# Kernel optimization log

Measured on AMD Instinct MI355X. Metric: run time of the kernel, lower is better.

The kernel has to match this reference:

```python
import jax, jax.numpy as jnp
import numpy as np
import math

N, E, D, H, EH, DEPTH = 50000, 800000, 128, 128, 16, 3
RATIO = 0.5
BN_SCALE = 1.0 / math.sqrt(1.0 + 1e-5)  # eval-mode BatchNorm1d: running mean 0, var 1
NEG_SLOPE = 0.01  # leaky_relu default


def setup_inputs() -> dict:
    key = jax.random.key(0)
    ks = jax.random.split(key, 16)
    s = lambda k, shape: jax.random.normal(k, shape, dtype=jnp.float32) * 0.05
    return {
        "x": jax.random.normal(ks[0], (N, D), dtype=jnp.float32),
        "edge_index": jax.random.randint(ks[1], (2, E), 0, N, dtype=jnp.int32),
        "edge_attr": jax.random.uniform(ks[2], (E, EH), dtype=jnp.float32),
        "We_w": s(ks[3], (EH, 1)), "We_b": s(ks[4], (1,)),
        "Wdown": s(ks[5], (DEPTH + 1, H, H)), "bdown": s(ks[6], (DEPTH + 1, H)),
        "Wpool": s(ks[7], (DEPTH, H)),
        "Wup": s(ks[8], (DEPTH, H, H)), "bup": s(ks[9], (DEPTH, H)),
        "gnorm": 1.0 + s(ks[10], (DEPTH + 1, H)), "bnorm": s(ks[11], (DEPTH + 1, H)),
        "Wr": s(ks[12], (D, D)), "br": s(ks[13], (D,)),
        "gr": 1.0 + s(ks[14], (D,)), "brn": s(ks[15], (D,)),
    }


def _bn(x, g, b):
    # eval-mode BatchNorm1d with running_mean=0, running_var=1
    return x * (g * BN_SCALE) + b


def _lrelu(x):
    return jnp.where(x > 0, x, NEG_SLOPE * x)


def _gcn(x, src, dst, w, W, b, fill):
    # PyG GCNConv: add self-loops (fill=1.0, improved -> 2.0), symmetric norm
    n = x.shape[0]
    h = x @ W  # [n, H]
    deg = jax.ops.segment_sum(w, dst, num_segments=n) + fill
    dinv = jax.lax.rsqrt(deg)
    coef = dinv[src] * w * dinv[dst]  # [E]
    agg = jax.ops.segment_sum(coef[:, None] * h[src], dst, num_segments=n)
    return agg + (fill / deg)[:, None] * h + b  # self-loop norm = fill/deg


def _topk_pool(x, src, dst, w, p, k):
    # PyG TopKPooling: score = tanh(x.p/||p||), keep top-k, scale kept x by score,
    # filter edges to kept nodes (masked edges kept at fixed length with weight 0)
    n = x.shape[0]
    score = jnp.tanh((x @ p) / jnp.linalg.norm(p))
    vals, perm = jax.lax.top_k(score, k)
    xp = x[perm] * vals[:, None]
    pos = jnp.full((n,), -1, dtype=jnp.int32).at[perm].set(jnp.arange(k, dtype=jnp.int32))
    ns, nd = pos[src], pos[dst]
    valid = (ns >= 0) & (nd >= 0)
    return (xp, jnp.where(valid, ns, 0), jnp.where(valid, nd, 0),
            jnp.where(valid, w, 0.0), perm)


def reference(x, edge_index, edge_attr, We_w, We_b, Wdown, bdown, Wpool, Wup, bup,
              gnorm, bnorm, Wr, br, gr, brn):
    src, dst = edge_index[0], edge_index[1]
    # edge embedding + min/max normalization
    ew = edge_attr @ We_w[:, 0] + We_b[0]  # [E]
    ew = ew - jnp.min(ew)
    ew = ew / (jnp.max(ew) + 1e-7)
    h = _bn(x, gnorm[0], bnorm[0])
    h = _lrelu(_gcn(h, src, dst, ew, Wdown[0], bdown[0], 1.0))
    xs, es, perms = [h], [(src, dst, ew)], []
    for i in range(DEPTH):
        k = int(math.ceil(RATIO * h.shape[0]))
        h, src, dst, ew, perm = _topk_pool(h, src, dst, ew, Wpool[i], k)
        h = _bn(h, gnorm[i + 1], bnorm[i + 1])
        h = _gcn(h, src, dst, ew, Wdown[i + 1], bdown[i + 1], 1.0)
        if i < DEPTH - 1:
            h = _lrelu(h)
            xs.append(h)
            es.append((src, dst, ew))
        perms.append(perm)
    for i in range(DEPTH):
        j = DEPTH - 1 - i
        res = xs[j]
        src, dst, ew = es[j]
        up = jnp.zeros_like(res).at[perms[j]].set(h)  # scatter unpool
        h = _gcn(res + up, src, dst, ew, Wup[i], bup[i], 2.0)  # improved=True -> fill 2
        if i < DEPTH - 1:
            h = _lrelu(h)
    g = jnp.sum(h, axis=0, keepdims=True)  # global_add_pool, single graph
    g = g @ Wr + br
    return _bn(g, gr, brn)
```

## Files before the change

kernel.cpp:

```cpp
#include <hip/hip_runtime.h>
#include <math.h>

#define N0   50000
#define E0   800000
#define HD   128
#define EHD  16
#define KP1  25000
#define KP2  12500
#define KP3  6250
#define BN_SCALE 0.9999950000374997f
#define NEG_SLOPE 0.01f
#define E1C  400000
#define E2C  120000
#define E3C  40000
#define NBE  782
#define CSB  782

#define NBIN   782
#define EPB    6144
#define NBLK   131
#define NBINP  784

typedef int   vi4 __attribute__((ext_vector_type(4)));
typedef float vf4 __attribute__((ext_vector_type(4)));

__device__ __forceinline__ unsigned fenc(float f) {
    unsigned u = __float_as_uint(f);
    return (u & 0x80000000u) ? ~u : (u | 0x80000000u);
}
__device__ __forceinline__ unsigned packbf2(float a, float b) {
    unsigned ua = __float_as_uint(a);
    unsigned ub = __float_as_uint(b);
    ua = (ua + 0x7FFFu + ((ua >> 16) & 1u)) >> 16;
    ub = (ub + 0x7FFFu + ((ub >> 16) & 1u)) >> 16;
    return ua | (ub << 16);
}
__device__ __forceinline__ void bf8_fma(float* acc, uint4 h, float c) {
    acc[0] += c * __uint_as_float(h.x << 16);
    acc[1] += c * __uint_as_float(h.x & 0xFFFF0000u);
    acc[2] += c * __uint_as_float(h.y << 16);
    acc[3] += c * __uint_as_float(h.y & 0xFFFF0000u);
    acc[4] += c * __uint_as_float(h.z << 16);
    acc[5] += c * __uint_as_float(h.z & 0xFFFF0000u);
    acc[6] += c * __uint_as_float(h.w << 16);
    acc[7] += c * __uint_as_float(h.w & 0xFFFF0000u);
}

__global__ void k_edge_ew(const float* __restrict__ ea, const float* __restrict__ Ww,
                          const float* __restrict__ Wb, float* __restrict__ ew,
                          float2* __restrict__ partials, int E) {
    int e = blockIdx.x * 256 + threadIdx.x;
    float mn = 3.4e38f, mx = -3.4e38f;
    if (e < E) {
        const float4* a4 = (const float4*)(ea + (size_t)e * EHD);
        float s = Wb[0];
        #pragma unroll
        for (int q = 0; q < 4; ++q) {
            float4 a = a4[q];
            s += a.x * Ww[q*4+0] + a.y * Ww[q*4+1] + a.z * Ww[q*4+2] + a.w * Ww[q*4+3];
        }
        ew[e] = s;
        mn = s; mx = s;
    }
    #pragma unroll
    for (int off = 32; off > 0; off >>= 1) {
        mn = fminf(mn, __shfl_xor(mn, off));
        mx = fmaxf(mx, __shfl_xor(mx, off));
    }
    __shared__ float smn[4], smx[4];
    int lane = threadIdx.x & 63, wid = threadIdx.x >> 6;
    if (lane == 0) { smn[wid] = mn; smx[wid] = mx; }
    __syncthreads();
    if (threadIdx.x == 0) {
        float a = fminf(fminf(smn[0], smn[1]), fminf(smn[2], smn[3]));
        float b = fmaxf(fmaxf(smx[0], smx[1]), fmaxf(smx[2], smx[3]));
        partials[blockIdx.x] = make_float2(a, b);
    }
}

__global__ void __launch_bounds__(1024)
k_reduce_mm(const float2* __restrict__ partials, int nb, float* __restrict__ mmv) {
    float mn = 3.4e38f, mx = -3.4e38f;
    for (int i = threadIdx.x; i < nb; i += 1024) {
        float2 t = partials[i];
        mn = fminf(mn, t.x); mx = fmaxf(mx, t.y);
    }
    #pragma unroll
    for (int off = 32; off > 0; off >>= 1) {
        mn = fminf(mn, __shfl_xor(mn, off));
        mx = fmaxf(mx, __shfl_xor(mx, off));
    }
    __shared__ float smn[16], smx[16];
    int lane = threadIdx.x & 63, wid = threadIdx.x >> 6;
    if (lane == 0) { smn[wid] = mn; smx[wid] = mx; }
    __syncthreads();
    if (threadIdx.x == 0) {
        for (int w = 1; w < 16; ++w) { mn = fminf(mn, smn[w]); mx = fmaxf(mx, smx[w]); }
        mmv[0] = mn; mmv[1] = mx;
    }
}

__global__ void __launch_bounds__(1024)
k_ew_sortA(float* __restrict__ ew, const float* __restrict__ mmv,
           const int* __restrict__ src, const int* __restrict__ dst,
           uint2* __restrict__ staging, int* __restrict__ cntM,
           int* __restrict__ locOffM, int E) {
    __shared__ uint2 sEnt[EPB];
    __shared__ int   lhist[NBINP];
    __shared__ int   sOff[NBINP];
    __shared__ int   lcur[NBINP];
    __shared__ int   wtot[16];
    int t = threadIdx.x;
    for (int i = t; i < NBINP; i += 1024) lhist[i] = 0;
    __syncthreads();
    float mn = mmv[0];
    float sc = 1.0f / ((mmv[1] - mn) + 1e-7f);
    int base = blockIdx.x * EPB;
    unsigned entx[6], enty[6];
    int bin6[6];
    #pragma unroll
    for (int it = 0; it < 6; ++it) {
        int e = base + it * 1024 + t;
        bin6[it] = -1;
        if (e < E) {
            float w = (ew[e] - mn) * sc;
            ew[e] = w;
            if (w != 0.0f) {
                int d = dst[e];
                bin6[it] = d >> 6;
                entx[it] = (unsigned)src[e] | ((unsigned)(d & 63) << 16);
                enty[it] = __float_as_uint(w);
                atomicAdd(&lhist[bin6[it]], 1);
            }
        }
    }
    __syncthreads();
    {
        int v = (t < NBINP) ? lhist[t] : 0;
        int lane = t & 63, wid = t >> 6;
        int x = v;
        #pragma unroll
        for (int off = 1; off < 64; off <<= 1) {
            int y = __shfl_up(x, off);
            if (lane >= off) x += y;
        }
        if (lane == 63) wtot[wid] = x;
        __syncthreads();
        int wb = 0;
        for (int w = 0; w < wid; ++w) wb += wtot[w];
        int excl = wb + x - v;
        if (t < NBINP) { sOff[t] = excl; lcur[t] = excl; }
    }
    __syncthreads();
    #pragma unroll
    for (int it = 0; it < 6; ++it) {
        if (bin6[it] >= 0) {
            int slot = atomicAdd(&lcur[bin6[it]], 1);
            sEnt[slot] = make_uint2(entx[it], enty[it]);
        }
    }
    __syncthreads();
    int total = sOff[NBIN];
    uint2* dstS = staging + (size_t)blockIdx.x * EPB;
    for (int i = t; i < total; i += 1024) dstS[i] = sEnt[i];
    int* cRow = cntM + blockIdx.x * NBINP;
    int* oRow = locOffM + blockIdx.x * NBINP;
    for (int i = t; i < NBINP; i += 1024) { cRow[i] = lhist[i]; oRow[i] = sOff[i]; }
}

__global__ void __launch_bounds__(1024)
k_bin_scan2(const int* __restrict__ cntM, int* __restrict__ binBase,
            int* __restrict__ rowptrEnd) {
    int t = threadIdx.x;
    int v = 0;
    if (t < NBIN) {
        for (int blk = 0; blk < NBLK; ++blk) v += cntM[blk * NBINP + t];
    }
    int lane = t & 63, wid = t >> 6;
    int xs = v;
    #pragma unroll
    for (int off = 1; off < 64; off <<= 1) {
        int y = __shfl_up(xs, off);
        if (lane >= off) xs += y;
    }
    __shared__ int wsum[16];
    if (lane == 63) wsum[wid] = xs;
    __syncthreads();
    int wb = 0;
    for (int w = 0; w < wid; ++w) wb += wsum[w];
    int excl = wb + xs - v;
    if (t < NBIN) binBase[t] = excl;
    if (t == NBIN - 1) rowptrEnd[0] = excl + v;
}

__global__ void __launch_bounds__(256)
k_binB2(const int* __restrict__ binBase, const int* __restrict__ cntM,
        const int* __restrict__ locOffM, const uint2* __restrict__ staging,
        int2* __restrict__ csr, float* __restrict__ sumW,
        int* __restrict__ rowptr, int n) {
    __shared__ uint2 raw[2048];
    __shared__ int   lhist[64];
    __shared__ int   lcur[64];
    __shared__ float lw[64];
    __shared__ int2  img[2048];
    __shared__ int   wq[4];
    __shared__ int   totalSh;
    int b = blockIdx.x;
    int t = threadIdx.x;
    int base = binBase[b];
    int c = 0, lo = 0;
    if (t < NBLK) { c = cntM[t * NBINP + b]; lo = locOffM[t * NBINP + b]; }
    int lane = t & 63, wid = t >> 6;
    int x = c;
    #pragma unroll
    for (int off = 1; off < 64; off <<= 1) {
        int y = __shfl_up(x, off);
        if (lane >= off) x += y;
    }
    if (lane == 63) wq[wid] = x;
    if (t < 64) { lhist[t] = 0; lw[t] = 0.f; }
    __syncthreads();
    int wb = 0;
    for (int w = 0; w < wid; ++w) wb += wq[w];
    int pos = wb + x - c;
    if (t == 255) totalSh = wb + x;
    __syncthreads();
    int total = min(totalSh, 2048);
    if (t < NBLK && c > 0) {
        const uint2* st = staging + (size_t)t * EPB + lo;
        for (int j = 0; j < c; ++j) {
            int p = pos + j;
            if (p < 2048) raw[p] = st[j];
        }
    }
    __syncthreads();
    for (int i = t; i < total; i += 256) {
        uint2 en = raw[i];
        int dloc = (en.x >> 16) & 63;
        atomicAdd(&lhist[dloc], 1);
        atomicAdd(&lw[dloc], __uint_as_float(en.y));
    }
    __syncthreads();
    if (t < 64) {
        int cc = lhist[t];
        int xs = cc;
        #pragma unroll
        for (int off = 1; off < 64; off <<= 1) {
            int y = __shfl_up(xs, off);
            if (t >= off) xs += y;
        }
        int excl = xs - cc;
        lcur[t] = excl;
        int v = b * 64 + t;
        if (v < n) { rowptr[v] = base + excl; sumW[v] = lw[t]; }
    }
    __syncthreads();
    for (int i = t; i < total; i += 256) {
        uint2 en = raw[i];
        int dloc = (en.x >> 16) & 63;
        int slot = atomicAdd(&lcur[dloc], 1);
        if (slot < 2048) img[slot] = make_int2((int)(en.x & 0xFFFFu), (int)en.y);
    }
    __syncthreads();
    for (int i = t; i < total; i += 256)
        csr[base + i] = img[i];
}

#define GT_ROWS 32
__global__ void __launch_bounds__(256)
k_gemm128(const float* __restrict__ A, const float* __restrict__ W,
          unsigned* __restrict__ Cb, int n,
          const float* __restrict__ gs, const float* __restrict__ gb,
          const float* __restrict__ up_h, const int* __restrict__ up_pos) {
    __shared__ float As[GT_ROWS][132];
    __shared__ float Ws[64][132];
    int tid = threadIdx.x;
    int row0 = blockIdx.x * GT_ROWS;
    int maxr = n - row0;
    {
        #pragma unroll
        for (int it = 0; it < 4; ++it) {
            int idx = it * 256 + tid;
            int r = idx >> 5, q = idx & 31;
            float4 v = make_float4(0.f, 0.f, 0.f, 0.f);
            if (r < maxr) {
                v = ((const float4*)(A + (size_t)(row0 + r) * HD))[q];
                if (up_pos) {
                    int sl = up_pos[row0 + r];
                    if (sl >= 0) {
                        float4 u = ((const float4*)(up_h + (size_t)sl * HD))[q];
                        v.x += u.x; v.y += u.y; v.z += u.z; v.w += u.w;
                    }
                }
                if (gs) {
                    float4 g4 = ((const float4*)gs)[q];
                    float4 b4 = ((const float4*)gb)[q];
                    v.x = v.x * (g4.x * BN_SCALE) + b4.x;
                    v.y = v.y * (g4.y * BN_SCALE) + b4.y;
                    v.z = v.z * (g4.z * BN_SCALE) + b4.z;
                    v.w = v.w * (g4.w * BN_SCALE) + b4.w;
                }
            }
            *(float4*)&As[r][q * 4] = v;
        }
    }
    int cg = tid & 31;
    int rg = tid >> 5;
    float4 acc[4];
    #pragma unroll
    for (int j = 0; j < 4; ++j) acc[j] = make_float4(0.f, 0.f, 0.f, 0.f);
    const float4* W4 = (const float4*)W;
    #pragma unroll
    for (int kb = 0; kb < HD; kb += 64) {
        __syncthreads();
        #pragma unroll
        for (int it = 0; it < 8; ++it) {
            int idx = it * 256 + tid;
            int r = idx >> 5, q = idx & 31;
            *(float4*)&Ws[r][q * 4] = W4[(size_t)(kb + r) * 32 + q];
        }
        __syncthreads();
        #pragma unroll 4
        for (int kk = 0; kk < 64; kk += 4) {
            float4 w0 = *(const float4*)&Ws[kk + 0][cg * 4];
            float4 w1 = *(const float4*)&Ws[kk + 1][cg * 4];
            float4 w2 = *(const float4*)&Ws[kk + 2][cg * 4];
            float4 w3 = *(const float4*)&Ws[kk + 3][cg * 4];
            #pragma unroll
            for (int jj = 0; jj < 4; ++jj) {
                float4 a = *(const float4*)&As[4 * rg + jj][kb + kk];
                acc[jj].x += a.x * w0.x + a.y * w1.x + a.z * w2.x + a.w * w3.x;
                acc[jj].y += a.x * w0.y + a.y * w1.y + a.z * w2.y + a.w * w3.y;
                acc[jj].z += a.x * w0.z + a.y * w1.z + a.z * w2.z + a.w * w3.z;
                acc[jj].w += a.x * w0.w + a.y * w1.w + a.z * w2.w + a.w * w3.w;
            }
        }
    }
    #pragma unroll
    for (int jj = 0; jj < 4; ++jj) {
        int r = 4 * rg + jj;
        if (r < maxr) {
            uint2 pk = make_uint2(packbf2(acc[jj].x, acc[jj].y), packbf2(acc[jj].z, acc[jj].w));
            ((uint2*)(Cb + (size_t)(row0 + r) * 64))[cg] = pk;
        }
    }
}

__global__ void k_sum_scan(const int* __restrict__ cnt, int* __restrict__ bsum, int n,
                           int* __restrict__ totalOut, unsigned* __restrict__ dctr) {
    int base = blockIdx.x * 1024;
    int s = 0;
    #pragma unroll
    for (int it = 0; it < 4; ++it) {
        int i = base + it * 256 + threadIdx.x;
        if (i < n) s += cnt[i];
    }
    __shared__ int ws[4];
    __shared__ int lastFlag;
    int lane = threadIdx.x & 63, wid = threadIdx.x >> 6;
    #pragma unroll
    for (int off = 32; off > 0; off >>= 1) s += __shfl_down(s, off);
    if (lane == 0) ws[wid] = s;
    __syncthreads();
    if (threadIdx.x == 0) {
        __hip_atomic_store(&bsum[blockIdx.x], ws[0] + ws[1] + ws[2] + ws[3],
                           __ATOMIC_RELAXED, __HIP_MEMORY_SCOPE_AGENT);
        unsigned prev = __hip_atomic_fetch_add(dctr, 1u, __ATOMIC_ACQ_REL, __HIP_MEMORY_SCOPE_AGENT);
        lastFlag = (prev == gridDim.x - 1);
    }
    __syncthreads();
    if (!lastFlag) return;
    if (threadIdx.x < 64) {
        int nb = gridDim.x;
        int t = threadIdx.x;
        int v = (t < nb) ? __hip_atomic_load(&bsum[t], __ATOMIC_RELAXED, __HIP_MEMORY_SCOPE_AGENT) : 0;
        int x = v;
        #pragma unroll
        for (int off = 1; off < 64; off <<= 1) {
            int y = __shfl_up(x, off);
            if (t >= off) x += y;
        }
        if (t < nb) bsum[t] = x - v;
        if (t == nb - 1) totalOut[0] = x;
    }
    if (threadIdx.x == 0)
        __hip_atomic_store(dctr, 0u, __ATOMIC_RELAXED, __HIP_MEMORY_SCOPE_AGENT);
}

__global__ void k_chunk_scan(const int* __restrict__ cnt, const int* __restrict__ bo,
                             int* __restrict__ rowptr, int* __restrict__ cursor, int n) {
    __shared__ int wsum[4];
    __shared__ int running;
    int base = blockIdx.x * 1024;
    if (threadIdx.x == 0) running = bo[blockIdx.x];
    __syncthreads();
    int lane = threadIdx.x & 63, wid = threadIdx.x >> 6;
    #pragma unroll
    for (int it = 0; it < 4; ++it) {
        int i = base + it * 256 + threadIdx.x;
        int v = (i < n) ? cnt[i] : 0;
        int x = v;
        #pragma unroll
        for (int off = 1; off < 64; off <<= 1) {
            int y = __shfl_up(x, off);
            if (lane >= off) x += y;
        }
        if (lane == 63) wsum[wid] = x;
        __syncthreads();
        int wb = 0;
        for (int w = 0; w < wid; ++w) wb += wsum[w];
        int excl = running + wb + x - v;
        if (i < n) { rowptr[i] = excl; cursor[i] = excl; }
        __syncthreads();
        if (threadIdx.x == 0) running += wsum[0] + wsum[1] + wsum[2] + wsum[3];
        __syncthreads();
    }
}

__global__ void k_csr_fill(const int* __restrict__ src, const int* __restrict__ dst,
                           const float* __restrict__ w, int* __restrict__ cursor,
                           int2* __restrict__ csr,
                           const int* __restrict__ EinPtr, int EinImm) {
    int Ein = EinPtr ? EinPtr[0] : EinImm;
    int e = blockIdx.x * 256 + threadIdx.x;
    if (e >= Ein) return;
    float wv = w[e];
    if (wv == 0.0f) return;
    int slot = atomicAdd(&cursor[dst[e]], 1);
    csr[slot] = make_int2(src[e], __float_as_int(wv));
}

__global__ void k_deg_dinv(const int* __restrict__ rowptr, const int2* __restrict__ csr,
                           float fill, float* __restrict__ deg, float* __restrict__ dinv, int n) {
    int v = blockIdx.x * 256 + threadIdx.x;
    if (v >= n) return;
    float s = fill;
    int rs = rowptr[v], re = rowptr[v + 1];
    for (int j = rs; j < re; ++j) s += __int_as_float(csr[j].y);
    deg[v] = s;
    dinv[v] = rsqrtf(s);
}

__global__ void k_deg_dinv_d(const float* __restrict__ sumW, float fill,
                             float* __restrict__ deg, float* __restrict__ dinv, int n) {
    int v = blockIdx.x * 256 + threadIdx.x;
    if (v >= n) return;
    float s = fill + sumW[v];
    deg[v] = s;
    dinv[v] = rsqrtf(s);
}

__global__ void __launch_bounds__(256)
k_gcn_gather(const int* __restrict__ rowptr, const int2* __restrict__ csr,
             const float* __restrict__ deg, const float* __restrict__ dinv,
             const unsigned* __restrict__ hWb,
             const float* __restrict__ bias,
             float fill, int n, int lrelu, float* __restrict__ out) {
    int v = blockIdx.x * 4 + (threadIdx.x >> 6);
    int lane = threadIdx.x & 63;
    if (v >= n) return;
    int rs = rowptr[v], re = rowptr[v + 1];
    float dv = dinv[v];
    int quarter = lane >> 4;
    int qi = lane & 15;
    float acc[8];
    #pragma unroll
    for (int i = 0; i < 8; ++i) acc[i] = 0.f;
    for (int base = rs; base < re; base += 64) {
        int idx = base + lane;
        int s_r = 0; float c_r = 0.f;
        if (idx < re) {
            int2 ent = csr[idx];
            s_r = ent.x;
            c_r = dinv[s_r] * __int_as_float(ent.y) * dv;
        }
        int cnt = min(64, re - base);
        int groups = cnt >> 2;
        int t = 0;
        for (; t + 1 < groups; t += 2) {
            int j0 = 4 * t + quarter, j1 = j0 + 4;
            int   s0 = __shfl(s_r, j0); float c0 = __shfl(c_r, j0);
            int   s1 = __shfl(s_r, j1); float c1 = __shfl(c_r, j1);
            uint4 h0 = ((const uint4*)(hWb + (size_t)s0 * 64))[qi];
            uint4 h1 = ((const uint4*)(hWb + (size_t)s1 * 64))[qi];
            bf8_fma(acc, h0, c0);
            bf8_fma(acc, h1, c1);
        }
        for (; t < groups; ++t) {
            int j = 4 * t + quarter;
            int s = __shfl(s_r, j); float c = __shfl(c_r, j);
            uint4 h = ((const uint4*)(hWb + (size_t)s * 64))[qi];
            bf8_fma(acc, h, c);
        }
        int rem = cnt & 3;
        if (quarter < rem) {
            int j = groups * 4 + quarter;
            int s = __shfl(s_r, j); float c = __shfl(c_r, j);
            uint4 h = ((const uint4*)(hWb + (size_t)s * 64))[qi];
            bf8_fma(acc, h, c);
        }
    }
    #pragma unroll
    for (int i = 0; i < 8; ++i) {
        acc[i] += __shfl_xor(acc[i], 16);
        acc[i] += __shfl_xor(acc[i], 32);
    }
    if (quarter == 0) {
        uint4 hs = ((const uint4*)(hWb + (size_t)v * 64))[qi];
        float sc = fill / deg[v];
        float hv[8];
        hv[0] = __uint_as_float(hs.x << 16); hv[1] = __uint_as_float(hs.x & 0xFFFF0000u);
        hv[2] = __uint_as_float(hs.y << 16); hv[3] = __uint_as_float(hs.y & 0xFFFF0000u);
        hv[4] = __uint_as_float(hs.z << 16); hv[5] = __uint_as_float(hs.z & 0xFFFF0000u);
        hv[6] = __uint_as_float(hs.w << 16); hv[7] = __uint_as_float(hs.w & 0xFFFF0000u);
        float4 b0 = ((const float4*)bias)[2 * qi];
        float4 b1 = ((const float4*)bias)[2 * qi + 1];
        float o[8];
        o[0] = acc[0] + sc * hv[0] + b0.x;
        o[1] = acc[1] + sc * hv[1] + b0.y;
        o[2] = acc[2] + sc * hv[2] + b0.z;
        o[3] = acc[3] + sc * hv[3] + b0.w;
        o[4] = acc[4] + sc * hv[4] + b1.x;
        o[5] = acc[5] + sc * hv[5] + b1.y;
        o[6] = acc[6] + sc * hv[6] + b1.z;
        o[7] = acc[7] + sc * hv[7] + b1.w;
        if (lrelu) {
            #pragma unroll
            for (int i = 0; i < 8; ++i) o[i] = (o[i] > 0.f) ? o[i] : NEG_SLOPE * o[i];
        }
        float4* orow = (float4*)(out + (size_t)v * HD);
        orow[2 * qi]     = make_float4(o[0], o[1], o[2], o[3]);
        orow[2 * qi + 1] = make_float4(o[4], o[5], o[6], o[7]);
    }
}

__global__ void k_score(const float* __restrict__ x, const float* __restrict__ p,
                        float* __restrict__ score, int n, int* __restrict__ selws) {
    for (int i = blockIdx.x * 256 + threadIdx.x; i < 5120; i += gridDim.x * 256) selws[i] = 0;
    int lane = threadIdx.x & 63;
    float pv0 = p[lane], pv1 = p[lane + 64];
    float ps = pv0 * pv0 + pv1 * pv1;
    #pragma unroll
    for (int off = 32; off > 0; off >>= 1) ps += __shfl_xor(ps, off);
    float rnorm = 1.0f / sqrtf(ps);
    int node = blockIdx.x * 4 + (threadIdx.x >> 6);
    if (node >= n) return;
    const float* row = x + (size_t)node * HD;
    float s = row[lane] * pv0 + row[lane + 64] * pv1;
    #pragma unroll
    for (int off = 32; off > 0; off >>= 1) s += __shfl_xor(s, off);
    if (lane == 0) score[node] = tanhf(s * rnorm);
}

__global__ void __launch_bounds__(256)
k_histpick(const float* __restrict__ score, int n, int pass,
           unsigned* __restrict__ prefix, int* __restrict__ hist,
           int kImm, const int* __restrict__ remIn, int* __restrict__ remOut,
           unsigned* __restrict__ doneCtr) {
    __shared__ int lh[2048];
    int nbins = (pass == 2) ? 1024 : 2048;
    for (int i = threadIdx.x; i < nbins; i += 256) lh[i] = 0;
    __syncthreads();
    unsigned pfx = (pass != 0) ? prefix[0] : 0u;
    int stride = gridDim.x * 256;
    for (int i = blockIdx.x * 256 + threadIdx.x; i < n; i += stride) {
        unsigned u = fenc(score[i]);
        int bin; bool ok;
        if (pass == 0)      { bin = u >> 21;            ok = true; }
        else if (pass == 1) { bin = (u >> 10) & 2047;   ok = ((u >> 21) == (pfx >> 21)); }
        else                { bin = u & 1023;           ok = ((u >> 10) == (pfx >> 10)); }
        if (ok) atomicAdd(&lh[bin], 1);
    }
    __syncthreads();
    for (int i = threadIdx.x; i < nbins; i += 256) {
        int c = lh[i];
        if (c) __hip_atomic_fetch_add(&hist[i], c, __ATOMIC_RELAXED, __HIP_MEMORY_SCOPE_AGENT);
    }
    __syncthreads();
    __shared__ int lastFlag;
    if (threadIdx.x == 0) {
        unsigned prev = __hip_atomic_fetch_add(doneCtr, 1u, __ATOMIC_ACQ_REL, __HIP_MEMORY_SCOPE_AGENT);
        lastFlag = (prev == gridDim.x - 1);
    }
    __syncthreads();
    if (!lastFlag) return;
    __shared__ int wsum[4];
    int k = remIn ? remIn[0] : kImm;
    int t = threadIdx.x;
    int per = nbins >> 8;
    int hi = nbins - t * per, lo = hi - per;
    int s = 0;
    for (int b = lo; b < hi; ++b)
        s += __hip_atomic_load(&hist[b], __ATOMIC_RELAXED, __HIP_MEMORY_SCOPE_AGENT);
    int lane = t & 63, wid = t >> 6;
    int x = s;
    #pragma unroll
    for (int off = 1; off < 64; off <<= 1) {
        int y = __shfl_up(x, off);
        if (lane >= off) x += y;
    }
    if (lane == 63) wsum[wid] = x;
    __syncthreads();
    int wb = 0;
    for (int w = 0; w < wid; ++w) wb += wsum[w];
    int excl = wb + x - s;
    if (k > excl && k <= excl + s) {
        int cum = excl;
        int shift = (pass == 0) ? 21 : (pass == 1) ? 10 : 0;
        for (int b = hi - 1; b >= lo; --b) {
            int h = __hip_atomic_load(&hist[b], __ATOMIC_RELAXED, __HIP_MEMORY_SCOPE_AGENT);
            if (k <= cum + h) {
                unsigned base = (pass == 0) ? 0u : prefix[0];
                prefix[0] = base | ((unsigned)b << shift);
                remOut[0] = k - cum;
                break;
            }
            cum += h;
        }
    }
    __syncthreads();
    if (threadIdx.x == 0)
        __hip_atomic_store(doneCtr, 0u, __ATOMIC_RELAXED, __HIP_MEMORY_SCOPE_AGENT);
}

__global__ void k_cmp_countscan(const float* __restrict__ score, int n,
                                const unsigned* __restrict__ prefix,
                                int* __restrict__ bgt, int* __restrict__ beq,
                                unsigned* __restrict__ dctr) {
    unsigned T = prefix[0];
    int base = blockIdx.x * 1024;
    int gt = 0, eq = 0;
    #pragma unroll
    for (int it = 0; it < 4; ++it) {
        int i = base + it * 256 + threadIdx.x;
        if (i < n) {
            unsigned u = fenc(score[i]);
            gt += (u > T); eq += (u == T);
        }
    }
    __shared__ int sg[4], se[4];
    __shared__ int lastFlag;
    int lane = threadIdx.x & 63, wid = threadIdx.x >> 6;
    #pragma unroll
    for (int off = 32; off > 0; off >>= 1) { gt += __shfl_down(gt, off); eq += __shfl_down(eq, off); }
    if (lane == 0) { sg[wid] = gt; se[wid] = eq; }
    __syncthreads();
    if (threadIdx.x == 0) {
        __hip_atomic_store(&bgt[blockIdx.x], sg[0] + sg[1] + sg[2] + sg[3],
                           __ATOMIC_RELAXED, __HIP_MEMORY_SCOPE_AGENT);
        __hip_atomic_store(&beq[blockIdx.x], se[0] + se[1] + se[2] + se[3],
                           __ATOMIC_RELAXED, __HIP_MEMORY_SCOPE_AGENT);
        unsigned prev = __hip_atomic_fetch_add(dctr, 1u, __ATOMIC_ACQ_REL, __HIP_MEMORY_SCOPE_AGENT);
        lastFlag = (prev == gridDim.x - 1);
    }
    __syncthreads();
    if (!lastFlag) return;
    if (threadIdx.x < 64) {
        int nb = gridDim.x;
        int t = threadIdx.x;
        int va = (t < nb) ? __hip_atomic_load(&bgt[t], __ATOMIC_RELAXED, __HIP_MEMORY_SCOPE_AGENT) : 0;
        int vb = (t < nb) ? __hip_atomic_load(&beq[t], __ATOMIC_RELAXED, __HIP_MEMORY_SCOPE_AGENT) : 0;
        int xa = va, xb = vb;
        #pragma unroll
        for (int off = 1; off < 64; off <<= 1) {
            int ya = __shfl_up(xa, off), yb = __shfl_up(xb, off);
            if (t >= off) { xa += ya; xb += yb; }
        }
        if (t < nb) { bgt[t] = xa - va; beq[t] = xb - vb; }
    }
    if (threadIdx.x == 0)
        __hip_atomic_store(dctr, 0u, __ATOMIC_RELAXED, __HIP_MEMORY_SCOPE_AGENT);
}

__global__ void k_cmp_assign(const float* __restrict__ score, int n, int kcap,
                             const unsigned* __restrict__ prefix,
                             const int* __restrict__ selTies,
                             const int* __restrict__ bgt, const int* __restrict__ beq,
                             int* __restrict__ pos, int* __restrict__ perm,
                             float* __restrict__ vals) {
    unsigned T = prefix[0];
    int tiesNeed = selTies[0];
    __shared__ int wgt[4], weq[4];
    __shared__ int rgt, req;
    int base = blockIdx.x * 1024;
    if (threadIdx.x == 0) { rgt = bgt[blockIdx.x]; req = beq[blockIdx.x]; }
    __syncthreads();
    int lane = threadIdx.x & 63, wid = threadIdx.x >> 6;
    #pragma unroll
    for (int it = 0; it < 4; ++it) {
        int i = base + it * 256 + threadIdx.x;
        bool in = i < n;
        float sc = in ? score[i] : 0.f;
        unsigned u = in ? fenc(sc) : 0u;
        bool g = in && (u > T);
        bool e = in && (u == T);
        unsigned long long mg = __ballot(g), me = __ballot(e);
        int lgt = __popcll(mg & ((1ull << lane) - 1ull));
        int leq = __popcll(me & ((1ull << lane) - 1ull));
        if (lane == 0) { wgt[wid] = __popcll(mg); weq[wid] = __popcll(me); }
        __syncthreads();
        int wbg = 0, wbe = 0;
        for (int w = 0; w < wid; ++w) { wbg += wgt[w]; wbe += weq[w]; }
        int gtRank = rgt + wbg + lgt;
        int tieRank = req + wbe + leq;
        if (in) {
            int slot = -1;
            if (g) slot = gtRank + min(tieRank, tiesNeed);
            else if (e && tieRank < tiesNeed) slot = gtRank + tieRank;
            if (slot >= kcap) slot = -1;
            pos[i] = slot;
            if (slot >= 0) { perm[slot] = i; vals[slot] = sc; }
        }
        __syncthreads();
        if (threadIdx.x == 0) {
            rgt += wgt[0] + wgt[1] + wgt[2] + wgt[3];
            req += weq[0] + weq[1] + weq[2] + weq[3];
        }
        __syncthreads();
    }
}

__global__ void k_pool_bn(const float* __restrict__ x, const int* __restrict__ perm,
                          const float* __restrict__ vals, const float* __restrict__ g,
                          const float* __restrict__ b, float* __restrict__ out, int k) {
    int idx = blockIdx.x * 256 + threadIdx.x;
    if (idx >= k * HD) return;
    int slot = idx >> 7, c = idx & 127;
    int v = perm[slot];
    out[idx] = (x[(size_t)v * HD + c] * vals[slot]) * (g[c] * BN_SCALE) + b[c];
}

__global__ void k_ecompact_countscan(const int* __restrict__ src, const int* __restrict__ dst,
                                     const float* __restrict__ w, const int* __restrict__ pos,
                                     const int* __restrict__ EinPtr, int EinImm, int kNodes,
                                     int* __restrict__ bsumE, int* __restrict__ ecntOut,
                                     int* __restrict__ cnt, unsigned* __restrict__ dctr) {
    int Ein = EinPtr ? EinPtr[0] : EinImm;
    for (int i = blockIdx.x * 256 + threadIdx.x; i < kNodes; i += gridDim.x * 256) cnt[i] = 0;
    int base = blockIdx.x * 1024;
    int c = 0;
    #pragma unroll
    for (int it = 0; it < 4; ++it) {
        int e = base + it * 256 + threadIdx.x;
        if (e < Ein) {
            float wv = w[e];
            if (wv != 0.0f && pos[src[e]] >= 0 && pos[dst[e]] >= 0) ++c;
        }
    }
    __shared__ int ws[4];
    __shared__ int lastFlag;
    int lane = threadIdx.x & 63, wid = threadIdx.x >> 6;
    #pragma unroll
    for (int off = 32; off > 0; off >>= 1) c += __shfl_down(c, off);
    if (lane == 0) ws[wid] = c;
    __syncthreads();
    if (threadIdx.x == 0) {
        __hip_atomic_store(&bsumE[blockIdx.x], ws[0] + ws[1] + ws[2] + ws[3],
                           __ATOMIC_RELAXED, __HIP_MEMORY_SCOPE_AGENT);
        unsigned prev = __hip_atomic_fetch_add(dctr, 1u, __ATOMIC_ACQ_REL, __HIP_MEMORY_SCOPE_AGENT);
        lastFlag = (prev == gridDim.x - 1);
    }
    __syncthreads();
    if (!lastFlag) return;
    {
        __shared__ int wtot[4];
        int nb = gridDim.x;
        int t = threadIdx.x;
        int i0 = t * 4;
        int v0 = (i0 + 0 < nb) ? __hip_atomic_load(&bsumE[i0 + 0], __ATOMIC_RELAXED, __HIP_MEMORY_SCOPE_AGENT) : 0;
        int v1 = (i0 + 1 < nb) ? __hip_atomic_load(&bsumE[i0 + 1], __ATOMIC_RELAXED, __HIP_MEMORY_SCOPE_AGENT) : 0;
        int v2 = (i0 + 2 < nb) ? __hip_atomic_load(&bsumE[i0 + 2], __ATOMIC_RELAXED, __HIP_MEMORY_SCOPE_AGENT) : 0;
        int v3 = (i0 + 3 < nb) ? __hip_atomic_load(&bsumE[i0 + 3], __ATOMIC_RELAXED, __HIP_MEMORY_SCOPE_AGENT) : 0;
        int tot = v0 + v1 + v2 + v3;
        int x2 = tot;
        #pragma unroll
        for (int off = 1; off < 64; off <<= 1) {
            int y = __shfl_up(x2, off);
            if (lane >= off) x2 += y;
        }
        if (lane == 63) wtot[wid] = x2;
        __syncthreads();
        int wb = 0;
        for (int q = 0; q < wid; ++q) wb += wtot[q];
        int excl = wb + x2 - tot;
        if (i0 + 0 < nb) bsumE[i0 + 0] = excl;
        if (i0 + 1 < nb) bsumE[i0 + 1] = excl + v0;
        if (i0 + 2 < nb) bsumE[i0 + 2] = excl + v0 + v1;
        if (i0 + 3 < nb) bsumE[i0 + 3] = excl + v0 + v1 + v2;
        if (t == 255) ecntOut[0] = wtot[0] + wtot[1] + wtot[2] + wtot[3];
    }
    __syncthreads();
    if (threadIdx.x == 0)
        __hip_atomic_store(dctr, 0u, __ATOMIC_RELAXED, __HIP_MEMORY_SCOPE_AGENT);
}

__global__ void k_ecompact_assign(const int* __restrict__ src, const int* __restrict__ dst,
                                  const float* __restrict__ w, const int* __restrict__ pos,
                                  const int* __restrict__ EinPtr, int EinImm,
                                  const int* __restrict__ bsumE,
                                  int* __restrict__ nsrc, int* __restrict__ ndst,
                                  float* __restrict__ nw, int* __restrict__ cnt) {
    int Ein = EinPtr ? EinPtr[0] : EinImm;
    __shared__ int wcnt[4];
    __shared__ int running;
    if (threadIdx.x == 0) running = bsumE[blockIdx.x];
    __syncthreads();
    int base = blockIdx.x * 1024;
    int lane = threadIdx.x & 63, wid = threadIdx.x >> 6;
    #pragma unroll
    for (int it = 0; it < 4; ++it) {
        int e = base + it * 256 + threadIdx.x;
        bool valid = false; int ns = 0, nd = 0; float wv = 0.f;
        if (e < Ein) {
            wv = w[e];
            if (wv != 0.0f) {
                ns = pos[src[e]]; nd = pos[dst[e]];
                valid = (ns >= 0) && (nd >= 0);
            }
        }
        unsigned long long m = __ballot(valid);
        int r = __popcll(m & ((1ull << lane) - 1ull));
        if (lane == 0) wcnt[wid] = __popcll(m);
        __syncthreads();
        int wb = 0;
        for (int w2 = 0; w2 < wid; ++w2) wb += wcnt[w2];
        if (valid) {
            int slot = running + wb + r;
            nsrc[slot] = ns; ndst[slot] = nd; nw[slot] = wv;
            atomicAdd(&cnt[nd], 1);
        }
        __syncthreads();
        if (threadIdx.x == 0) running += wcnt[0] + wcnt[1] + wcnt[2] + wcnt[3];
        __syncthreads();
    }
}

__global__ void __launch_bounds__(256)
k_colsum_part(const float* __restrict__ h, float* __restrict__ cpart, int n) {
    int c = threadIdx.x & 127;
    int rh = threadIdx.x >> 7;
    int r0 = blockIdx.x * 64;
    int r1 = min(n, r0 + 64);
    float local = 0.f;
    for (int r = r0 + rh; r < r1; r += 2) local += h[(size_t)r * HD + c];
    __shared__ float sh[256];
    sh[threadIdx.x] = local;
    __syncthreads();
    if (threadIdx.x < 128) cpart[(size_t)blockIdx.x * HD + c] = sh[c] + sh[c + 128];
}

__global__ void __launch_bounds__(1024)
k_colsum_final(const float* __restrict__ cpart, int nb,
               const float* __restrict__ Wr, const float* __restrict__ br,
               const float* __restrict__ gr, const float* __restrict__ brn,
               float* __restrict__ out) {
    __shared__ float gsh[HD];
    int c = threadIdx.x & 127;
    int seg = threadIdx.x >> 7;
    float local = 0.f;
    for (int b = seg; b < nb; b += 8) local += cpart[(size_t)b * HD + c];
    __shared__ float sh[1024];
    sh[threadIdx.x] = local;
    __syncthreads();
    if (threadIdx.x < 128) {
        float s = 0.f;
        #pragma unroll
        for (int q = 0; q < 8; ++q) s += sh[c + q * 128];
        gsh[c] = s;
    }
    __syncthreads();
    if (threadIdx.x < 128) {
        float s = br[c];
        for (int k = 0; k < HD; ++k) s += gsh[k] * Wr[k * HD + c];
        out[c] = s * (gr[c] * BN_SCALE) + brn[c];
    }
}

extern "C" void kernel_launch(void* const* d_in, const int* in_sizes, int n_in,
                              void* d_out, int out_size, void* d_ws, size_t ws_size,
                              hipStream_t stream) {
    const float* x     = (const float*)d_in[0];
    const int*   ei    = (const int*)d_in[1];
    const float* eattr = (const float*)d_in[2];
    const float* We_w  = (const float*)d_in[3];
    const float* We_b  = (const float*)d_in[4];
    const float* Wdown = (const float*)d_in[5];
    const float* bdown = (const float*)d_in[6];
    const float* Wpool = (const float*)d_in[7];
    const float* Wup   = (const float*)d_in[8];
    const float* bup   = (const float*)d_in[9];
    const float* gnorm = (const float*)d_in[10];
    const float* bnorm = (const float*)d_in[11];
    const float* Wr    = (const float*)d_in[12];
    const float* br    = (const float*)d_in[13];
    const float* gr    = (const float*)d_in[14];
    const float* brn   = (const float*)d_in[15];
    const int* src0 = ei;
    const int* dst0 = ei + E0;
    float* out = (float*)d_out;

    char* p = (char*)d_ws;
    auto alloc = [&](size_t bytes) -> void* {
        void* r = (void*)p;
        p += (bytes + 255) & ~(size_t)255;
        return r;
    };
    float* ew0  = (float*)alloc(E0 * 4);
    int* src1 = (int*)alloc(E1C * 4); int* dst1 = (int*)alloc(E1C * 4); float* ew1 = (float*)alloc(E1C * 4);
    int* src2 = (int*)alloc(E2C * 4); int* dst2 = (int*)alloc(E2C * 4); float* ew2 = (float*)alloc(E2C * 4);
    int* src3 = (int*)alloc(E3C * 4); int* dst3 = (int*)alloc(E3C * 4); float* ew3 = (float*)alloc(E3C * 4);
    float* hbuf = (float*)alloc((size_t)N0 * HD * 4);
    unsigned* hWb = (unsigned*)alloc((size_t)N0 * 64 * 4);
    float* tmp  = (float*)alloc((size_t)N0 * HD * 4);
    float* xs0  = (float*)alloc((size_t)N0 * HD * 4);
    float* xs1  = (float*)alloc((size_t)KP1 * HD * 4);
    float* xs2  = (float*)alloc((size_t)KP2 * HD * 4);
    float* deg   = (float*)alloc(N0 * 4);
    float* dinv  = (float*)alloc(N0 * 4);
    float* sumW0 = (float*)alloc(N0 * 4);
    float* score = (float*)alloc(N0 * 4);
    int*   pos1  = (int*)alloc(N0 * 4);
    int*   pos2  = (int*)alloc(N0 * 4);
    int*   pos3  = (int*)alloc(N0 * 4);
    float* vals  = (float*)alloc(KP1 * 4);
    int* perm1 = (int*)alloc(KP1 * 4);
    int* perm2 = (int*)alloc(KP2 * 4);
    int* perm3 = (int*)alloc(KP3 * 4);
    int* rowptr0 = (int*)alloc((N0 + 1) * 4);
    int* rowptr1 = (int*)alloc((KP1 + 1) * 4);
    int* rowptr2 = (int*)alloc((KP2 + 1) * 4);
    int* rowptr3 = (int*)alloc((KP3 + 1) * 4);
    int2* csrP0 = (int2*)alloc((size_t)E0 * 8);
    int2* csrP1 = (int2*)alloc((size_t)E1C * 8);
    int2* csrP2 = (int2*)alloc((size_t)E2C * 8);
    int2* csrP3 = (int2*)alloc((size_t)E3C * 8);
    int* cnt    = (int*)alloc(N0 * 4);
    int* cursor = (int*)alloc(N0 * 4);
    int* selws  = (int*)alloc(5120 * 4);
    int* hist0 = selws;
    int* hist1 = selws + 2048;
    int* hist2 = selws + 4096;
    int* bgt    = (int*)alloc(64 * 4);
    int* beq    = (int*)alloc(64 * 4);
    int* bsum   = (int*)alloc(64 * 4);
    int* bsumE  = (int*)alloc(1024 * 4);
    float2* partials = (float2*)alloc(((E0 + 255) / 256) * 8);
    float* cpart = (float*)alloc((size_t)CSB * HD * 4);
    float* mmv       = (float*)alloc(64);
    unsigned* ctrws  = (unsigned*)alloc(64 * 4);
    unsigned* dctrS  = ctrws + 0;
    unsigned* dctrH  = ctrws + 8;
    unsigned* dctrC  = ctrws + 16;
    unsigned* dctrE  = ctrws + 24;
    unsigned* prefix = (unsigned*)alloc(64);
    int* rem0        = (int*)alloc(64);
    int* rem1        = (int*)alloc(64);
    int* tiesN       = (int*)alloc(64);
    int* ecnt1       = (int*)alloc(64);
    int* ecnt2       = (int*)alloc(64);
    int* ecnt3       = (int*)alloc(64);
    int* cntM        = (int*)alloc((size_t)NBLK * NBINP * 4);
    int* locOffM     = (int*)alloc((size_t)NBLK * NBINP * 4);
    int* binBase     = (int*)alloc((NBIN + 1) * 4);
    uint2* staging   = (uint2*)tmp;

    const int EB = (E0 + 255) / 256;

    auto build_csr = [&](const int* esrc, const int* edst, const float* eww, int n,
                         int* rowptr, int2* csrP,
                         const int* EinPtr, int EinImm, int gridE) {
        int nb = (n + 1023) / 1024;
        k_sum_scan<<<nb, 256, 0, stream>>>(cnt, bsum, n, rowptr + n, dctrS);
        k_chunk_scan<<<nb, 256, 0, stream>>>(cnt, bsum, rowptr, cursor, n);
        k_csr_fill<<<gridE, 256, 0, stream>>>(esrc, edst, eww, cursor, csrP, EinPtr, EinImm);
    };

    auto run_gcn = [&](const float* hin, const int* rowptr, const int2* csrP,
                       const float* sumW,
                       const float* W, const float* bias, float fill, int n, int lrelu,
                       float* outbuf, const float* bn_g, const float* bn_b,
                       const float* up_h, const int* up_pos) {
        k_gemm128<<<(n + GT_ROWS - 1) / GT_ROWS, 256, 0, stream>>>(hin, W, hWb, n, bn_g, bn_b, up_h, up_pos);
        if (sumW)
            k_deg_dinv_d<<<(n + 255) / 256, 256, 0, stream>>>(sumW, fill, deg, dinv, n);
        else
            k_deg_dinv<<<(n + 255) / 256, 256, 0, stream>>>(rowptr, csrP, fill, deg, dinv, n);
        k_gcn_gather<<<(n + 3) / 4, 256, 0, stream>>>(rowptr, csrP, deg, dinv, hWb,
                                                      bias, fill, n, lrelu, outbuf);
    };

    auto run_pool = [&](const float* xin, int n, int k, const float* pvec,
                        const float* g, const float* b,
                        const int* esrc_in, const int* edst_in, const float* ew_in,
                        const int* EinPtr, int EinImm,
                        int* pos, int* perm,
                        int* esrc_out, int* edst_out, float* ew_out, int* ecntOut) {
        int nb = (n + 1023) / 1024;
        k_score<<<(n + 3) / 4, 256, 0, stream>>>(xin, pvec, score, n, selws);
        k_histpick<<<64, 256, 0, stream>>>(score, n, 0, prefix, hist0, k, (const int*)nullptr, rem0, dctrH);
        k_histpick<<<64, 256, 0, stream>>>(score, n, 1, prefix, hist1, 0, rem0, rem1, dctrH);
        k_histpick<<<64, 256, 0, stream>>>(score, n, 2, prefix, hist2, 0, rem1, tiesN, dctrH);
        k_cmp_countscan<<<nb, 256, 0, stream>>>(score, n, prefix, bgt, beq, dctrC);
        k_cmp_assign<<<nb, 256, 0, stream>>>(score, n, k, prefix, tiesN, bgt, beq, pos, perm, vals);
        k_pool_bn<<<((size_t)k * HD + 255) / 256, 256, 0, stream>>>(xin, perm, vals, g, b, hbuf, k);
        k_ecompact_countscan<<<NBE, 256, 0, stream>>>(esrc_in, edst_in, ew_in, pos, EinPtr, EinImm, k,
                                                      bsumE, ecntOut, cnt, dctrE);
        k_ecompact_assign<<<NBE, 256, 0, stream>>>(esrc_in, edst_in, ew_in, pos, EinPtr, EinImm,
                                                   bsumE, esrc_out, edst_out, ew_out, cnt);
    };

    hipMemsetAsync((void*)ctrws, 0, 64 * 4, stream);

    k_edge_ew<<<EB, 256, 0, stream>>>(eattr, We_w, We_b, ew0, partials, E0);
    k_reduce_mm<<<1, 1024, 0, stream>>>(partials, EB, mmv);
    k_ew_sortA<<<NBLK, 1024, 0, stream>>>(ew0, mmv, src0, dst0, staging, cntM, locOffM, E0);

    k_bin_scan2<<<1, 1024, 0, stream>>>(cntM, binBase, rowptr0 + N0);
    k_binB2<<<NBIN, 256, 0, stream>>>(binBase, cntM, locOffM, staging, csrP0, sumW0,
                                      rowptr0, N0);

    run_gcn(x, rowptr0, csrP0, sumW0, Wdown, bdown, 1.0f, N0, 1, xs0, gnorm, bnorm, nullptr, nullptr);

    run_pool(xs0, N0, KP1, Wpool, gnorm + HD, bnorm + HD, src0, dst0, ew0,
             (const int*)nullptr, E0, pos1, perm1, src1, dst1, ew1, ecnt1);
    build_csr(src1, dst1, ew1, KP1, rowptr1, csrP1, ecnt1, 0, (E1C + 255) / 256);
    run_gcn(hbuf, rowptr1, csrP1, nullptr, Wdown + 1 * HD * HD, bdown + 1 * HD, 1.0f, KP1, 1, xs1,
            nullptr, nullptr, nullptr, nullptr);

    run_pool(xs1, KP1, KP2, Wpool + HD, gnorm + 2 * HD, bnorm + 2 * HD, src1, dst1, ew1,
             ecnt1, 0, pos2, perm2, src2, dst2, ew2, ecnt2);
    build_csr(src2, dst2, ew2, KP2, rowptr2, csrP2, ecnt2, 0, (E2C + 255) / 256);
    run_gcn(hbuf, rowptr2, csrP2, nullptr, Wdown + 2 * HD * HD, bdown + 2 * HD, 1.0f, KP2, 1, xs2,
            nullptr, nullptr, nullptr, nullptr);

    run_pool(xs2, KP2, KP3, Wpool + 2 * HD, gnorm + 3 * HD, bnorm + 3 * HD, src2, dst2, ew2,
             ecnt2, 0, pos3, perm3, src3, dst3, ew3, ecnt3);
    build_csr(src3, dst3, ew3, KP3, rowptr3, csrP3, ecnt3, 0, (E3C + 255) / 256);
    run_gcn(hbuf, rowptr3, csrP3, nullptr, Wdown + 3 * HD * HD, bdown + 3 * HD, 1.0f, KP3, 0, tmp,
            nullptr, nullptr, nullptr, nullptr);

    run_gcn(xs2, rowptr2, csrP2, nullptr, Wup, bup, 2.0f, KP2, 1, tmp, nullptr, nullptr, tmp, pos3);

    run_gcn(xs1, rowptr1, csrP1, nullptr, Wup + 1 * HD * HD, bup + 1 * HD, 2.0f, KP1, 1, tmp,
            nullptr, nullptr, tmp, pos2);

    run_gcn(xs0, rowptr0, csrP0, sumW0, Wup + 2 * HD * HD, bup + 2 * HD, 2.0f, N0, 0, tmp,
            nullptr, nullptr, tmp, pos1);

    k_colsum_part<<<CSB, 256, 0, stream>>>(tmp, cpart, N0);
    k_colsum_final<<<1, 1024, 0, stream>>>(cpart, CSB, Wr, br, gr, brn, out);
}
```

Baseline: 796.5 us.

## Replace scalar FP32 GEMM with bf16 MFMA GEMM using pre-transposed bf16 weights

```diff
diff --git a/kernel.cpp b/kernel.cpp
--- a/kernel.cpp
+++ b/kernel.cpp
@@ -23,6 +23,8 @@
 
 typedef int   vi4 __attribute__((ext_vector_type(4)));
 typedef float vf4 __attribute__((ext_vector_type(4)));
+typedef __bf16 bfrag8 __attribute__((ext_vector_type(8)));
+typedef float  f32x4  __attribute__((ext_vector_type(4)));
 
 __device__ __forceinline__ unsigned fenc(float f) {
     unsigned u = __float_as_uint(f);
@@ -266,82 +268,130 @@
         csr[base + i] = img[i];
 }
 
-#define GT_ROWS 32
 __global__ void __launch_bounds__(256)
-k_gemm128(const float* __restrict__ A, const float* __restrict__ W,
+k_wconv(const float* __restrict__ Wsrc, unsigned* __restrict__ WbT) {
+    __shared__ ushort Wl[128][136];
+    const float* W = Wsrc + (size_t)blockIdx.x * HD * HD;
+    unsigned* Wo = WbT + (size_t)blockIdx.x * HD * 64;
+    int tid = threadIdx.x;
+    #pragma unroll
+    for (int it = 0; it < 16; ++it) {
+        int idx = it * 256 + tid;
+        int k = idx >> 5, c4 = (idx & 31) * 4;
+        float4 v = ((const float4*)(W + (size_t)k * HD))[idx & 31];
+        Wl[c4 + 0][k] = (ushort)packbf2(v.x, 0.f);
+        Wl[c4 + 1][k] = (ushort)packbf2(v.y, 0.f);
+        Wl[c4 + 2][k] = (ushort)packbf2(v.z, 0.f);
+        Wl[c4 + 3][k] = (ushort)packbf2(v.w, 0.f);
+    }
+    __syncthreads();
+    #pragma unroll
+    for (int it = 0; it < 16; ++it) {
+        int idx = it * 256 + tid;
+        int c = idx >> 5, j = idx & 31;
+        uint2 o;
+        o.x = (unsigned)Wl[c][4*j + 0] | ((unsigned)Wl[c][4*j + 1] << 16);
+        o.y = (unsigned)Wl[c][4*j + 2] | ((unsigned)Wl[c][4*j + 3] << 16);
+        ((uint2*)Wo)[c * 32 + j] = o;
+    }
+}
+
+#define GT_ROWS 64
+#define APAD 136
+__global__ void __launch_bounds__(256)
+k_gemm_mf(const float* __restrict__ A, const unsigned* __restrict__ WbT,
           unsigned* __restrict__ Cb, int n,
           const float* __restrict__ gs, const float* __restrict__ gb,
           const float* __restrict__ up_h, const int* __restrict__ up_pos) {
-    __shared__ float As[GT_ROWS][132];
-    __shared__ float Ws[64][132];
+    __shared__ char ldsb[(64 + 128) * APAD * 2];
+    ushort (*Al)[APAD] = (ushort(*)[APAD])ldsb;
+    ushort (*Wl)[APAD] = (ushort(*)[APAD])(ldsb + 64 * APAD * 2);
+    float  (*outS)[132] = (float(*)[132])ldsb;
     int tid = threadIdx.x;
     int row0 = blockIdx.x * GT_ROWS;
     int maxr = n - row0;
-    {
-        #pragma unroll
-        for (int it = 0; it < 4; ++it) {
-            int idx = it * 256 + tid;
-            int r = idx >> 5, q = idx & 31;
-            float4 v = make_float4(0.f, 0.f, 0.f, 0.f);
-            if (r < maxr) {
-                v = ((const float4*)(A + (size_t)(row0 + r) * HD))[q];
-                if (up_pos) {
-                    int sl = up_pos[row0 + r];
-                    if (sl >= 0) {
-                        float4 u = ((const float4*)(up_h + (size_t)sl * HD))[q];
-                        v.x += u.x; v.y += u.y; v.z += u.z; v.w += u.w;
-                    }
-                }
-                if (gs) {
-                    float4 g4 = ((const float4*)gs)[q];
-                    float4 b4 = ((const float4*)gb)[q];
-                    v.x = v.x * (g4.x * BN_SCALE) + b4.x;
-                    v.y = v.y * (g4.y * BN_SCALE) + b4.y;
-                    v.z = v.z * (g4.z * BN_SCALE) + b4.z;
-                    v.w = v.w * (g4.w * BN_SCALE) + b4.w;
+    #pragma unroll
+    for (int it = 0; it < 8; ++it) {
+        int idx = it * 256 + tid;
+        int r = idx >> 5, q = idx & 31;
+        float4 v = make_float4(0.f, 0.f, 0.f, 0.f);
+        if (r < maxr) {
+            v = ((const float4*)(A + (size_t)(row0 + r) * HD))[q];
+            if (up_pos) {
+                int sl = up_pos[row0 + r];
+                if (sl >= 0) {
+                    float4 u = ((const float4*)(up_h + (size_t)sl * HD))[q];
+                    v.x += u.x; v.y += u.y; v.z += u.z; v.w += u.w;
                 }
             }
-            *(float4*)&As[r][q * 4] = v;
-        }
-    }
-    int cg = tid & 31;
-    int rg = tid >> 5;
-    float4 acc[4];
-    #pragma unroll
-    for (int j = 0; j < 4; ++j) acc[j] = make_float4(0.f, 0.f, 0.f, 0.f);
-    const float4* W4 = (const float4*)W;
-    #pragma unroll
-    for (int kb = 0; kb < HD; kb += 64) {
-        __syncthreads();
-        #pragma unroll
-        for (int it = 0; it < 8; ++it) {
-            int idx = it * 256 + tid;
-            int r = idx >> 5, q = idx & 31;
-            *(float4*)&Ws[r][q * 4] = W4[(size_t)(kb + r) * 32 + q];
-        }
-        __syncthreads();
-        #pragma unroll 4
-        for (int kk = 0; kk < 64; kk += 4) {
-            float4 w0 = *(const float4*)&Ws[kk + 0][cg * 4];
-            float4 w1 = *(const float4*)&Ws[kk + 1][cg * 4];
-            float4 w2 = *(const float4*)&Ws[kk + 2][cg * 4];
-            float4 w3 = *(const float4*)&Ws[kk + 3][cg * 4];
+            if (gs) {
+                float4 g4 = ((const float4*)gs)[q];
+                float4 b4 = ((const float4*)gb)[q];
+                v.x = v.x * (g4.x * BN_SCALE) + b4.x;
+                v.y = v.y * (g4.y * BN_SCALE) + b4.y;
+                v.z = v.z * (g4.z * BN_SCALE) + b4.z;
+                v.w = v.w * (g4.w * BN_SCALE) + b4.w;
+            }
+        }
+        uint2 pk = make_uint2(packbf2(v.x, v.y), packbf2(v.z, v.w));
+        *(uint2*)&Al[r][q * 4] = pk;
+    }
+    #pragma unroll
+    for (int it = 0; it < 16; ++it) {
+        int idx = it * 256 + tid;
+        int c = idx >> 5, j = idx & 31;
+        uint2 wv = ((const uint2*)WbT)[c * 32 + j];
+        *(uint2*)&Wl[c][j * 4] = wv;
+    }
+    __syncthreads();
+    int lane = tid & 63;
+    int w = tid >> 6;
+    int r0 = (w & 1) * 32;
+    int c0 = (w >> 1) * 64;
+    int fr = lane & 15;
+    int fg = lane >> 4;
+    bfrag8 af[2][4];
+    #pragma unroll
+    for (int rt = 0; rt < 2; ++rt)
+        #pragma unroll
+        for (int ks = 0; ks < 4; ++ks)
+            af[rt][ks] = *(const bfrag8*)&Al[r0 + rt * 16 + fr][ks * 32 + fg * 8];
+    f32x4 acc[2][4];
+    #pragma unroll
+    for (int rt = 0; rt < 2; ++rt)
+        #pragma unroll
+        for (int ct = 0; ct < 4; ++ct)
+            acc[rt][ct] = (f32x4)(0.f);
+    #pragma unroll
+    for (int ct = 0; ct < 4; ++ct) {
+        bfrag8 bf[4];
+        #pragma unroll
+        for (int ks = 0; ks < 4; ++ks)
+            bf[ks] = *(const bfrag8*)&Wl[c0 + ct * 16 + fr][ks * 32 + fg * 8];
+        #pragma unroll
+        for (int rt = 0; rt < 2; ++rt)
             #pragma unroll
-            for (int jj = 0; jj < 4; ++jj) {
-                float4 a = *(const float4*)&As[4 * rg + jj][kb + kk];
-                acc[jj].x += a.x * w0.x + a.y * w1.x + a.z * w2.x + a.w * w3.x;
-                acc[jj].y += a.x * w0.y + a.y * w1.y + a.z * w2.y + a.w * w3.y;
-                acc[jj].z += a.x * w0.z + a.y * w1.z + a.z * w2.z + a.w * w3.z;
-                acc[jj].w += a.x * w0.w + a.y * w1.w + a.z * w2.w + a.w * w3.w;
-            }
-        }
-    }
-    #pragma unroll
-    for (int jj = 0; jj < 4; ++jj) {
-        int r = 4 * rg + jj;
+            for (int ks = 0; ks < 4; ++ks)
+                acc[rt][ct] = __builtin_amdgcn_mfma_f32_16x16x32_bf16(
+                    af[rt][ks], bf[ks], acc[rt][ct], 0, 0, 0);
+    }
+    __syncthreads();
+    #pragma unroll
+    for (int rt = 0; rt < 2; ++rt)
+        #pragma unroll
+        for (int ct = 0; ct < 4; ++ct)
+            #pragma unroll
+            for (int r = 0; r < 4; ++r)
+                outS[r0 + rt * 16 + fg * 4 + r][c0 + ct * 16 + fr] = acc[rt][ct][r];
+    __syncthreads();
+    #pragma unroll
+    for (int it = 0; it < 8; ++it) {
+        int idx = it * 256 + tid;
+        int r = idx >> 5, q = idx & 31;
         if (r < maxr) {
-            uint2 pk = make_uint2(packbf2(acc[jj].x, acc[jj].y), packbf2(acc[jj].z, acc[jj].w));
-            ((uint2*)(Cb + (size_t)(row0 + r) * 64))[cg] = pk;
+            float4 o = *(const float4*)&outS[r][q * 4];
+            uint2 pk = make_uint2(packbf2(o.x, o.y), packbf2(o.z, o.w));
+            ((uint2*)(Cb + (size_t)(row0 + r) * 64))[q] = pk;
         }
     }
 }
@@ -963,6 +1013,8 @@
     int* locOffM     = (int*)alloc((size_t)NBLK * NBINP * 4);
     int* binBase     = (int*)alloc((NBIN + 1) * 4);
     uint2* staging   = (uint2*)tmp;
+    unsigned* WbtD   = (unsigned*)alloc((size_t)7 * HD * 64 * 4);
+    unsigned* WbtU   = WbtD + (size_t)4 * HD * 64;
 
     const int EB = (E0 + 255) / 256;
 
@@ -977,10 +1029,10 @@
 
     auto run_gcn = [&](const float* hin, const int* rowptr, const int2* csrP,
                        const float* sumW,
-                       const float* W, const float* bias, float fill, int n, int lrelu,
+                       const unsigned* WbT, const float* bias, float fill, int n, int lrelu,
                        float* outbuf, const float* bn_g, const float* bn_b,
                        const float* up_h, const int* up_pos) {
-        k_gemm128<<<(n + GT_ROWS - 1) / GT_ROWS, 256, 0, stream>>>(hin, W, hWb, n, bn_g, bn_b, up_h, up_pos);
+        k_gemm_mf<<<(n + GT_ROWS - 1) / GT_ROWS, 256, 0, stream>>>(hin, WbT, hWb, n, bn_g, bn_b, up_h, up_pos);
         if (sumW)
             k_deg_dinv_d<<<(n + 255) / 256, 256, 0, stream>>>(sumW, fill, deg, dinv, n);
         else
@@ -1011,6 +1063,9 @@
 
     hipMemsetAsync((void*)ctrws, 0, 64 * 4, stream);
 
+    k_wconv<<<4, 256, 0, stream>>>(Wdown, WbtD);
+    k_wconv<<<3, 256, 0, stream>>>(Wup, WbtU);
+
     k_edge_ew<<<EB, 256, 0, stream>>>(eattr, We_w, We_b, ew0, partials, E0);
     k_reduce_mm<<<1, 1024, 0, stream>>>(partials, EB, mmv);
     k_ew_sortA<<<NBLK, 1024, 0, stream>>>(ew0, mmv, src0, dst0, staging, cntM, locOffM, E0);
@@ -1019,32 +1074,32 @@
     k_binB2<<<NBIN, 256, 0, stream>>>(binBase, cntM, locOffM, staging, csrP0, sumW0,
                                       rowptr0, N0);
 
-    run_gcn(x, rowptr0, csrP0, sumW0, Wdown, bdown, 1.0f, N0, 1, xs0, gnorm, bnorm, nullptr, nullptr);
+    run_gcn(x, rowptr0, csrP0, sumW0, WbtD, bdown, 1.0f, N0, 1, xs0, gnorm, bnorm, nullptr, nullptr);
 
     run_pool(xs0, N0, KP1, Wpool, gnorm + HD, bnorm + HD, src0, dst0, ew0,
              (const int*)nullptr, E0, pos1, perm1, src1, dst1, ew1, ecnt1);
     build_csr(src1, dst1, ew1, KP1, rowptr1, csrP1, ecnt1, 0, (E1C + 255) / 256);
-    run_gcn(hbuf, rowptr1, csrP1, nullptr, Wdown + 1 * HD * HD, bdown + 1 * HD, 1.0f, KP1, 1, xs1,
+    run_gcn(hbuf, rowptr1, csrP1, nullptr, WbtD + 1 * HD * 64, bdown + 1 * HD, 1.0f, KP1, 1, xs1,
             nullptr, nullptr, nullptr, nullptr);
 
     run_pool(xs1, KP1, KP2, Wpool + HD, gnorm + 2 * HD, bnorm + 2 * HD, src1, dst1, ew1,
              ecnt1, 0, pos2, perm2, src2, dst2, ew2, ecnt2);
     build_csr(src2, dst2, ew2, KP2, rowptr2, csrP2, ecnt2, 0, (E2C + 255) / 256);
-    run_gcn(hbuf, rowptr2, csrP2, nullptr, Wdown + 2 * HD * HD, bdown + 2 * HD, 1.0f, KP2, 1, xs2,
+    run_gcn(hbuf, rowptr2, csrP2, nullptr, WbtD + 2 * HD * 64, bdown + 2 * HD, 1.0f, KP2, 1, xs2,
             nullptr, nullptr, nullptr, nullptr);
 
     run_pool(xs2, KP2, KP3, Wpool + 2 * HD, gnorm + 3 * HD, bnorm + 3 * HD, src2, dst2, ew2,
              ecnt2, 0, pos3, perm3, src3, dst3, ew3, ecnt3);
     build_csr(src3, dst3, ew3, KP3, rowptr3, csrP3, ecnt3, 0, (E3C + 255) / 256);
-    run_gcn(hbuf, rowptr3, csrP3, nullptr, Wdown + 3 * HD * HD, bdown + 3 * HD, 1.0f, KP3, 0, tmp,
+    run_gcn(hbuf, rowptr3, csrP3, nullptr, WbtD + 3 * HD * 64, bdown + 3 * HD, 1.0f, KP3, 0, tmp,
             nullptr, nullptr, nullptr, nullptr);
 
-    run_gcn(xs2, rowptr2, csrP2, nullptr, Wup, bup, 2.0f, KP2, 1, tmp, nullptr, nullptr, tmp, pos3);
-
-    run_gcn(xs1, rowptr1, csrP1, nullptr, Wup + 1 * HD * HD, bup + 1 * HD, 2.0f, KP1, 1, tmp,
+    run_gcn(xs2, rowptr2, csrP2, nullptr, WbtU, bup, 2.0f, KP2, 1, tmp, nullptr, nullptr, tmp, pos3);
+
+    run_gcn(xs1, rowptr1, csrP1, nullptr, WbtU + 1 * HD * 64, bup + 1 * HD, 2.0f, KP1, 1, tmp,
             nullptr, nullptr, tmp, pos2);
 
-    run_gcn(xs0, rowptr0, csrP0, sumW0, Wup + 2 * HD * HD, bup + 2 * HD, 2.0f, N0, 0, tmp,
+    run_gcn(xs0, rowptr0, csrP0, sumW0, WbtU + 2 * HD * 64, bup + 2 * HD, 2.0f, N0, 0, tmp,
             nullptr, nullptr, tmp, pos1);
 
     k_colsum_part<<<CSB, 256, 0, stream>>>(tmp, cpart, N0);
```

Result: faster. 720.8 us (-9.5%).
